# Performance work log

Hardware: AMD Instinct MI355X
Metric: run time of the kernel (lower is better)

Reference implementation:

```python
import jax, jax.numpy as jnp
import numpy as np

# Static part-graph structure (matches adj_matrix in init_kwargs; torch.nonzero row-major order)
ADJ = np.array([[0,1,0,0,0,0],
                [1,0,1,1,1,1],
                [0,1,0,0,0,0],
                [0,1,0,0,0,0],
                [0,1,0,0,0,0],
                [0,1,0,0,0,0]], dtype=np.int64)
_EDGES = np.argwhere(ADJ)            # [E,2] = (src, dst)
SRC = jnp.asarray(_EDGES[:, 0])
DST = jnp.asarray(_EDGES[:, 1])
NUM_PARTS = 6
# parts 1..4 are upper (use xh[0]), parts 5..6 lower (use xh[1])
HALVES = jnp.array([0, 0, 0, 0, 1, 1])


def setup_inputs() -> dict:
    key = jax.random.key(0)
    ks = jax.random.split(key, 12)
    B, H, W, Cin, h, P = 16, 96, 96, 256, 10, NUM_PARTS
    s = 0.05  # weight scale
    return {
        "p_fea":    jax.random.normal(ks[0], (B, Cin, H, W), jnp.float32),
        "xp_stack": jax.random.normal(ks[1], (P, B, h, H, W), jnp.float32),
        "xh_stack": jax.random.normal(ks[2], (2, B, h, H, W), jnp.float32),
        "w_att":  jax.random.normal(ks[3], (P, h), jnp.float32) * s,      # grouped 1x1 conv (groups=P)
        "b_att":  jnp.zeros((P,), jnp.float32),
        "w_dp_f": jax.random.normal(ks[4], (h, Cin), jnp.float32) * s,    # Part_Dependency: p_fea branch
        "w_dp_x": jax.random.normal(ks[5], (h, h), jnp.float32) * s,      # Part_Dependency: xp branch
        "b_dp":   jnp.zeros((h,), jnp.float32),
        "w_proj": jax.random.normal(ks[6], (P, h, Cin), jnp.float32) * s, # Decomposition proj (per part)
        "b_proj": jnp.zeros((P, h), jnp.float32),
        "w_gate": jax.random.normal(ks[7], (P, 2 * h), jnp.float32) * s,  # Decomposition gate on cat(xh,xp)
        "b_gate": jnp.zeros((P,), jnp.float32),
        "w_upd":  jax.random.normal(ks[8], (P, h, 3 * h), jnp.float32) * s,  # att_Update on cat(xp,xpp,xhp)
        "b_upd":  jnp.zeros((P, h), jnp.float32),
    }


def reference(p_fea, xp_stack, xh_stack, w_att, b_att, w_dp_f, w_dp_x, b_dp,
              w_proj, b_proj, w_gate, b_gate, w_upd, b_upd):
    # xp_stack: [P,B,h,H,W], p_fea: [B,Cin,H,W]
    P = xp_stack.shape[0]

    # grouped 1x1 conv + sigmoid -> per-part attention map [P,B,1,H,W]
    att = jax.nn.sigmoid(jnp.einsum('pbchw,pc->pbhw', xp_stack, w_att)
                         + b_att[:, None, None, None])[:, :, None]

    # Part_Dependency: dp_i = relu(W_f @ p_fea + W_x @ xp_i + b), shared weights -> [P,B,h,H,W]
    dp = jax.nn.relu(jnp.einsum('bchw,dc->bdhw', p_fea, w_dp_f)[None]
                     + jnp.einsum('pbchw,dc->pbdhw', xp_stack, w_dp_x)
                     + b_dp[None, None, :, None, None])

    # Pair_Part_Dependency per edge: sigmoid-gated fusion, then sum-aggregate at dst
    msg = att[SRC] * att[DST] * (dp[SRC] + xp_stack[DST])   # [E,B,h,H,W]
    xpp = jax.ops.segment_sum(msg, DST, num_segments=P)     # [P,B,h,H,W]

    # Decomposition: gate half-body feature onto a projection of p_fea (per-part weights)
    xh_sel = xh_stack[HALVES]                                # [P,B,h,H,W]
    proj = jnp.einsum('bchw,pdc->pbdhw', p_fea, w_proj) + b_proj[:, None, :, None, None]
    gate = jax.nn.sigmoid(jnp.einsum('pbchw,pc->pbhw',
                                     jnp.concatenate([xh_sel, xp_stack], axis=2), w_gate)
                          + b_gate[:, None, None, None])[:, :, None]
    xhp = gate * proj                                        # [P,B,h,H,W]

    # att_Update: residual update from cat(xp, xpp, xhp) via per-part 1x1 conv
    cat3 = jnp.concatenate([xp_stack, xpp, xhp], axis=2)     # [P,B,3h,H,W]
    xp_out = xp_stack + jax.nn.relu(jnp.einsum('pbchw,pdc->pbdhw', cat3, w_upd)
                                    + b_upd[:, None, :, None, None])
    return xp_out, xpp, xhp
```

## Files before the change

kernel.cpp:

```cpp
#include <hip/hip_runtime.h>

#define HWSZ 9216
#define CIN  256
#define NPER 8847360
#define PSTRIDE 1474560
#define IMG_STRIDE 2359296
#define BHW 92160

#define OFF_WATT  18432
#define OFF_BATT  18492
#define OFF_WDPX  18498
#define OFF_BDP   18598
#define OFF_BPROJ 18608
#define OFF_WGATE 18668
#define OFF_BGATE 18788
#define OFF_WUPD  18794
#define OFF_BUPD  20594
#define WS_TOTAL  20654
#define A_OFF_U16 41472
#define A_ELEMS   20480

typedef __attribute__((ext_vector_type(8))) short short8;
typedef __attribute__((ext_vector_type(4))) float f32x4;
typedef __attribute__((ext_vector_type(4))) float flt4;

static __device__ __forceinline__ unsigned short f2b(float f) {
  union { float f; unsigned int i; } v; v.f = f;
  unsigned int u = v.i;
  return (unsigned short)((u + 0x7fffu + ((u >> 16) & 1u)) >> 16);
}
static __device__ __forceinline__ float sigmoidf_(float x) {
  return 1.0f / (1.0f + __expf(-x));
}

__global__ void prep_weights(const float* __restrict__ w_att,
                             const float* __restrict__ b_att,
                             const float* __restrict__ w_dp_f,
                             const float* __restrict__ w_dp_x,
                             const float* __restrict__ b_dp,
                             const float* __restrict__ w_proj,
                             const float* __restrict__ b_proj,
                             const float* __restrict__ w_gate,
                             const float* __restrict__ b_gate,
                             const float* __restrict__ w_upd,
                             const float* __restrict__ b_upd,
                             float* __restrict__ ws)
{
  int i = blockIdx.x * 256 + threadIdx.x;
  if (i < A_ELEMS) {
    int j     = i & 7;
    int lane  = (i >> 3) & 63;
    int kstep = (i >> 9) & 7;
    int mtile = i >> 12;
    int m = mtile * 16 + (lane & 15);
    int k = kstep * 32 + ((lane >> 4) & 3) * 8 + j;
    float wv = (m < 10) ? w_dp_f[m * CIN + k]
             : (m < 70) ? w_proj[(m - 10) * CIN + k] : 0.f;
    ((unsigned short*)ws)[A_OFF_U16 + i] = f2b(wv);
  }
  if (i >= WS_TOTAL || i < OFF_WATT) return;
  float v;
  if      (i < OFF_BATT)  v = w_att [i - OFF_WATT ];
  else if (i < OFF_WDPX)  v = b_att [i - OFF_BATT ];
  else if (i < OFF_BDP)   v = w_dp_x[i - OFF_WDPX ];
  else if (i < OFF_BPROJ) v = b_dp  [i - OFF_BDP  ];
  else if (i < OFF_WGATE) v = b_proj[i - OFF_BPROJ];
  else if (i < OFF_BGATE) v = w_gate[i - OFF_WGATE];
  else if (i < OFF_WUPD)  v = b_gate[i - OFF_BGATE];
  else if (i < OFF_BUPD)  v = w_upd [i - OFF_WUPD ];
  else                    v = b_upd [i - OFF_BUPD ];
  ws[i] = v;
}

static __device__ __forceinline__ void epilogue1(
    int px, int p, int b, int s0,
    const float* __restrict__ xp, const float* __restrict__ xh,
    const float* __restrict__ ws,
    float* __restrict__ S, float* __restrict__ dpL,
    float* __restrict__ attL, float* __restrict__ gateL)
{
  const size_t base = (size_t)b * BHW + s0 + px;
  const float* xpb = xp + (size_t)p * PSTRIDE + base;
  const float* xhb = xh + (size_t)(p >= 4 ? 1 : 0) * PSTRIDE + base;
  float asum = ws[OFF_BATT + p], gsum = ws[OFF_BGATE + p];
  float xpv[10];
#pragma unroll
  for (int ch = 0; ch < 10; ++ch) {
    float x  = xpb[(size_t)ch * HWSZ];
    float hv = xhb[(size_t)ch * HWSZ];
    xpv[ch] = x;
    asum = fmaf(ws[OFF_WATT + p * 10 + ch], x, asum);
    gsum = fmaf(ws[OFF_WGATE + p * 20 + 10 + ch], x, gsum);
    gsum = fmaf(ws[OFF_WGATE + p * 20 + ch], hv, gsum);
  }
  attL [p * 64 + px] = sigmoidf_(asum);
  gateL[p * 64 + px] = sigmoidf_(gsum);
#pragma unroll
  for (int ch = 0; ch < 10; ++ch) {
    float t = S[ch * 72 + px] + ws[OFF_BDP + ch];
#pragma unroll
    for (int j = 0; j < 10; ++j) t = fmaf(ws[OFF_WDPX + ch * 10 + j], xpv[j], t);
    dpL[(p * 10 + ch) * 64 + px] = fmaxf(t, 0.f);
  }
}

static __device__ __forceinline__ void epilogue2(
    int px, int p, int b, int s0,
    const float* __restrict__ xp, const float* __restrict__ ws,
    const float* __restrict__ S, const float* __restrict__ dpL,
    const float* __restrict__ attL, const float* __restrict__ gateL,
    float* __restrict__ out)
{
  const size_t base = (size_t)b * BHW + s0 + px;
  const float* xpb = xp + (size_t)p * PSTRIDE + base;
  float xpv[10], xppv[10], xhpv[10];
#pragma unroll
  for (int ch = 0; ch < 10; ++ch) xpv[ch] = xpb[(size_t)ch * HWSZ];
  float att1 = attL[64 + px];
  if (p == 1) {
    float sA = 0.f;
#pragma unroll
    for (int q = 0; q < 6; ++q) if (q != 1) sA += attL[q * 64 + px];
#pragma unroll
    for (int ch = 0; ch < 10; ++ch) {
      float s1 = 0.f;
#pragma unroll
      for (int q = 0; q < 6; ++q)
        if (q != 1) s1 = fmaf(attL[q * 64 + px], dpL[(q * 10 + ch) * 64 + px], s1);
      xppv[ch] = att1 * fmaf(sA, xpv[ch], s1);
    }
  } else {
    float aa = att1 * attL[p * 64 + px];
#pragma unroll
    for (int ch = 0; ch < 10; ++ch)
      xppv[ch] = aa * (dpL[(10 + ch) * 64 + px] + xpv[ch]);
  }
  float g = gateL[p * 64 + px];
#pragma unroll
  for (int ch = 0; ch < 10; ++ch)
    xhpv[ch] = g * (S[(10 + p * 10 + ch) * 72 + px] + ws[OFF_BPROJ + p * 10 + ch]);
  float* o0 = out + (size_t)p * PSTRIDE + base;
#pragma unroll
  for (int ch = 0; ch < 10; ++ch) {
    float u = ws[OFF_BUPD + p * 10 + ch];
    const float* wu = ws + OFF_WUPD + (p * 10 + ch) * 30;
#pragma unroll
    for (int j = 0; j < 10; ++j) u = fmaf(wu[j],      xpv[j],  u);
#pragma unroll
    for (int j = 0; j < 10; ++j) u = fmaf(wu[10 + j], xppv[j], u);
#pragma unroll
    for (int j = 0; j < 10; ++j) u = fmaf(wu[20 + j], xhpv[j], u);
    u = fmaxf(u, 0.f);
    o0[(size_t)ch * HWSZ]                    = xpv[ch] + u;
    o0[(size_t)ch * HWSZ + NPER]             = xppv[ch];
    o0[(size_t)ch * HWSZ + 2 * (size_t)NPER] = xhpv[ch];
  }
}

__global__ __launch_bounds__(256) void part_graph_main(
    const float* __restrict__ p_fea,
    const float* __restrict__ xp,
    const float* __restrict__ xh,
    const float* __restrict__ ws,
    float* __restrict__ out)
{
  __shared__ __align__(16) char smem[38592];
  unsigned short* Bt = (unsigned short*)smem;
  float* S     = (float*)smem;
  float* dpL   = (float*)(smem + 20160);
  float* attL  = (float*)(smem + 35520);
  float* gateL = (float*)(smem + 37056);

  const int tid = threadIdx.x;
  const int b   = blockIdx.x / 144;
  const int s0  = (blockIdx.x % 144) * 64;

  {
    const int lane16 = tid & 15;
    const int cslot  = tid >> 4;
    const float* fb = p_fea + (size_t)b * IMG_STRIDE + s0 + lane16 * 4;
    const int nb = lane16 * 4;
#pragma unroll 4
    for (int it = 0; it < 16; ++it) {
      int c = cslot + it * 16;
      flt4 v = *(const flt4*)(fb + (size_t)c * HWSZ);
      Bt[(nb + 0) * 264 + c] = f2b(v.x);
      Bt[(nb + 1) * 264 + c] = f2b(v.y);
      Bt[(nb + 2) * 264 + c] = f2b(v.z);
      Bt[(nb + 3) * 264 + c] = f2b(v.w);
    }
  }
  __syncthreads();

  const int wv   = tid >> 6;
  const int lane = tid & 63;
  const int l15  = lane & 15;
  const int quad = lane >> 4;

  short8 bfrag[8];
  {
    const unsigned short* bp = Bt + (wv * 16 + l15) * 264 + quad * 8;
#pragma unroll
    for (int ks = 0; ks < 8; ++ks)
      bfrag[ks] = *(const short8*)(bp + ks * 32);
  }
  __syncthreads();

  f32x4 acc[5];
  const short8* ap = (const short8*)((const unsigned short*)ws + A_OFF_U16);
#pragma unroll
  for (int mt = 0; mt < 5; ++mt) {
    f32x4 a = {0.f, 0.f, 0.f, 0.f};
#pragma unroll
    for (int ks = 0; ks < 8; ++ks) {
      short8 af = ap[(mt * 8 + ks) * 64 + lane];
      a = __builtin_amdgcn_mfma_f32_16x16x32_bf16(af, bfrag[ks], a, 0, 0, 0);
    }
    acc[mt] = a;
  }

#pragma unroll
  for (int mt = 0; mt < 5; ++mt) {
#pragma unroll
    for (int r = 0; r < 4; ++r) {
      int m = mt * 16 + quad * 4 + r;
      if (m < 70) S[m * 72 + wv * 16 + l15] = acc[mt][r];
    }
  }
  __syncthreads();

  { int px = tid & 63, p = tid >> 6;
    epilogue1(px, p, b, s0, xp, xh, ws, S, dpL, attL, gateL); }
  if (tid < 128) {
    int px = tid & 63, p = 4 + (tid >> 6);
    epilogue1(px, p, b, s0, xp, xh, ws, S, dpL, attL, gateL);
  }
  __syncthreads();

  { int px = tid & 63, p = tid >> 6;
    epilogue2(px, p, b, s0, xp, ws, S, dpL, attL, gateL, out); }
  if (tid < 128) {
    int px = tid & 63, p = 4 + (tid >> 6);
    epilogue2(px, p, b, s0, xp, ws, S, dpL, attL, gateL, out);
  }
}

extern "C" void kernel_launch(void* const* d_in, const int* in_sizes, int n_in,
                              void* d_out, int out_size, void* d_ws, size_t ws_size,
                              hipStream_t stream) {
  const float* p_fea = (const float*)d_in[0];
  const float* xp    = (const float*)d_in[1];
  const float* xh    = (const float*)d_in[2];
  float* ws = (float*)d_ws;

  prep_weights<<<(WS_TOTAL + 255) / 256, 256, 0, stream>>>(
      (const float*)d_in[3],  (const float*)d_in[4],
      (const float*)d_in[5],  (const float*)d_in[6],
      (const float*)d_in[7],  (const float*)d_in[8],
      (const float*)d_in[9],  (const float*)d_in[10],
      (const float*)d_in[11], (const float*)d_in[12],
      (const float*)d_in[13], ws);

  part_graph_main<<<2304, 256, 0, stream>>>(
      p_fea, xp, xh, ws, (float*)d_out);
}
```

Baseline: 335.3 us.

## Load p_fea directly into MFMA fragments and restructure epilogue with paired pixels

Drops the shared-memory transpose of p_fea: each lane loads its B-fragment straight from global memory, converts it to bf16 and issues the MFMAs inline. The epilogue now has one thread handle two adjacent pixels for a single part, with 192 threads active. Each xp/xh value is loaded once and kept in registers across both phases instead of being re-read from global memory. The part-1 aggregation is reduced into shared memory with atomics rather than storing all per-part dp maps, which shrinks LDS and allows an occupancy hint of 6 blocks per SM. The risks are strided, uncoalesced global loads for the fragments, LDS atomics, and a quarter of the threads sitting idle in the epilogue.

After: 723.6 us. 116% more time.

```diff
diff --git a/kernel.cpp b/kernel.cpp
--- a/kernel.cpp
+++ b/kernel.cpp
@@ -22,7 +22,16 @@
 
 typedef __attribute__((ext_vector_type(8))) short short8;
 typedef __attribute__((ext_vector_type(4))) float f32x4;
-typedef __attribute__((ext_vector_type(4))) float flt4;
+typedef __attribute__((ext_vector_type(2))) float f32x2;
+
+#define SS     66
+#define L_S    0
+#define L_DP1  4620
+#define L_S1   5280
+#define L_SA   5940
+#define L_ATT  6008
+#define L_GATE 6392
+#define L_TOT  6776
 
 static __device__ __forceinline__ unsigned short f2b(float f) {
   union { float f; unsigned int i; } v; v.f = f;
@@ -72,151 +81,43 @@
   ws[i] = v;
 }
 
-static __device__ __forceinline__ void epilogue1(
-    int px, int p, int b, int s0,
-    const float* __restrict__ xp, const float* __restrict__ xh,
-    const float* __restrict__ ws,
-    float* __restrict__ S, float* __restrict__ dpL,
-    float* __restrict__ attL, float* __restrict__ gateL)
-{
-  const size_t base = (size_t)b * BHW + s0 + px;
-  const float* xpb = xp + (size_t)p * PSTRIDE + base;
-  const float* xhb = xh + (size_t)(p >= 4 ? 1 : 0) * PSTRIDE + base;
-  float asum = ws[OFF_BATT + p], gsum = ws[OFF_BGATE + p];
-  float xpv[10];
-#pragma unroll
-  for (int ch = 0; ch < 10; ++ch) {
-    float x  = xpb[(size_t)ch * HWSZ];
-    float hv = xhb[(size_t)ch * HWSZ];
-    xpv[ch] = x;
-    asum = fmaf(ws[OFF_WATT + p * 10 + ch], x, asum);
-    gsum = fmaf(ws[OFF_WGATE + p * 20 + 10 + ch], x, gsum);
-    gsum = fmaf(ws[OFF_WGATE + p * 20 + ch], hv, gsum);
-  }
-  attL [p * 64 + px] = sigmoidf_(asum);
-  gateL[p * 64 + px] = sigmoidf_(gsum);
-#pragma unroll
-  for (int ch = 0; ch < 10; ++ch) {
-    float t = S[ch * 72 + px] + ws[OFF_BDP + ch];
-#pragma unroll
-    for (int j = 0; j < 10; ++j) t = fmaf(ws[OFF_WDPX + ch * 10 + j], xpv[j], t);
-    dpL[(p * 10 + ch) * 64 + px] = fmaxf(t, 0.f);
-  }
-}
-
-static __device__ __forceinline__ void epilogue2(
-    int px, int p, int b, int s0,
-    const float* __restrict__ xp, const float* __restrict__ ws,
-    const float* __restrict__ S, const float* __restrict__ dpL,
-    const float* __restrict__ attL, const float* __restrict__ gateL,
-    float* __restrict__ out)
-{
-  const size_t base = (size_t)b * BHW + s0 + px;
-  const float* xpb = xp + (size_t)p * PSTRIDE + base;
-  float xpv[10], xppv[10], xhpv[10];
-#pragma unroll
-  for (int ch = 0; ch < 10; ++ch) xpv[ch] = xpb[(size_t)ch * HWSZ];
-  float att1 = attL[64 + px];
-  if (p == 1) {
-    float sA = 0.f;
-#pragma unroll
-    for (int q = 0; q < 6; ++q) if (q != 1) sA += attL[q * 64 + px];
-#pragma unroll
-    for (int ch = 0; ch < 10; ++ch) {
-      float s1 = 0.f;
-#pragma unroll
-      for (int q = 0; q < 6; ++q)
-        if (q != 1) s1 = fmaf(attL[q * 64 + px], dpL[(q * 10 + ch) * 64 + px], s1);
-      xppv[ch] = att1 * fmaf(sA, xpv[ch], s1);
-    }
-  } else {
-    float aa = att1 * attL[p * 64 + px];
-#pragma unroll
-    for (int ch = 0; ch < 10; ++ch)
-      xppv[ch] = aa * (dpL[(10 + ch) * 64 + px] + xpv[ch]);
-  }
-  float g = gateL[p * 64 + px];
-#pragma unroll
-  for (int ch = 0; ch < 10; ++ch)
-    xhpv[ch] = g * (S[(10 + p * 10 + ch) * 72 + px] + ws[OFF_BPROJ + p * 10 + ch]);
-  float* o0 = out + (size_t)p * PSTRIDE + base;
-#pragma unroll
-  for (int ch = 0; ch < 10; ++ch) {
-    float u = ws[OFF_BUPD + p * 10 + ch];
-    const float* wu = ws + OFF_WUPD + (p * 10 + ch) * 30;
-#pragma unroll
-    for (int j = 0; j < 10; ++j) u = fmaf(wu[j],      xpv[j],  u);
-#pragma unroll
-    for (int j = 0; j < 10; ++j) u = fmaf(wu[10 + j], xppv[j], u);
-#pragma unroll
-    for (int j = 0; j < 10; ++j) u = fmaf(wu[20 + j], xhpv[j], u);
-    u = fmaxf(u, 0.f);
-    o0[(size_t)ch * HWSZ]                    = xpv[ch] + u;
-    o0[(size_t)ch * HWSZ + NPER]             = xppv[ch];
-    o0[(size_t)ch * HWSZ + 2 * (size_t)NPER] = xhpv[ch];
-  }
-}
-
-__global__ __launch_bounds__(256) void part_graph_main(
+__global__ __launch_bounds__(256, 6) void part_graph_main(
     const float* __restrict__ p_fea,
     const float* __restrict__ xp,
     const float* __restrict__ xh,
     const float* __restrict__ ws,
     float* __restrict__ out)
 {
-  __shared__ __align__(16) char smem[38592];
-  unsigned short* Bt = (unsigned short*)smem;
-  float* S     = (float*)smem;
-  float* dpL   = (float*)(smem + 20160);
-  float* attL  = (float*)(smem + 35520);
-  float* gateL = (float*)(smem + 37056);
+  __shared__ __align__(16) float smem[L_TOT];
 
   const int tid = threadIdx.x;
   const int b   = blockIdx.x / 144;
   const int s0  = (blockIdx.x % 144) * 64;
 
-  {
-    const int lane16 = tid & 15;
-    const int cslot  = tid >> 4;
-    const float* fb = p_fea + (size_t)b * IMG_STRIDE + s0 + lane16 * 4;
-    const int nb = lane16 * 4;
-#pragma unroll 4
-    for (int it = 0; it < 16; ++it) {
-      int c = cslot + it * 16;
-      flt4 v = *(const flt4*)(fb + (size_t)c * HWSZ);
-      Bt[(nb + 0) * 264 + c] = f2b(v.x);
-      Bt[(nb + 1) * 264 + c] = f2b(v.y);
-      Bt[(nb + 2) * 264 + c] = f2b(v.z);
-      Bt[(nb + 3) * 264 + c] = f2b(v.w);
-    }
-  }
-  __syncthreads();
-
-  const int wv   = tid >> 6;
-  const int lane = tid & 63;
-  const int l15  = lane & 15;
-  const int quad = lane >> 4;
-
-  short8 bfrag[8];
-  {
-    const unsigned short* bp = Bt + (wv * 16 + l15) * 264 + quad * 8;
-#pragma unroll
-    for (int ks = 0; ks < 8; ++ks)
-      bfrag[ks] = *(const short8*)(bp + ks * 32);
-  }
-  __syncthreads();
+  for (int i = tid; i < 726; i += 256) smem[L_S1 + i] = 0.f;
+
+  const int lane = tid & 63, wv = tid >> 6;
+  const int l15  = lane & 15, quad = lane >> 4;
+  const float* pf = p_fea + (size_t)b * IMG_STRIDE + s0 + wv * 16 + l15
+                  + (size_t)quad * 8 * HWSZ;
+  const short8* ap = (const short8*)((const unsigned short*)ws + A_OFF_U16);
 
   f32x4 acc[5];
-  const short8* ap = (const short8*)((const unsigned short*)ws + A_OFF_U16);
-#pragma unroll
-  for (int mt = 0; mt < 5; ++mt) {
-    f32x4 a = {0.f, 0.f, 0.f, 0.f};
-#pragma unroll
-    for (int ks = 0; ks < 8; ++ks) {
-      short8 af = ap[(mt * 8 + ks) * 64 + lane];
-      a = __builtin_amdgcn_mfma_f32_16x16x32_bf16(af, bfrag[ks], a, 0, 0, 0);
-    }
-    acc[mt] = a;
+#pragma unroll
+  for (int mt = 0; mt < 5; ++mt) acc[mt] = (f32x4){0.f, 0.f, 0.f, 0.f};
+
+#pragma unroll
+  for (int ks = 0; ks < 8; ++ks) {
+    float t[8];
+#pragma unroll
+    for (int j = 0; j < 8; ++j) t[j] = pf[(size_t)(ks * 32 + j) * HWSZ];
+    short8 bf;
+#pragma unroll
+    for (int j = 0; j < 8; ++j) bf[j] = (short)f2b(t[j]);
+#pragma unroll
+    for (int mt = 0; mt < 5; ++mt)
+      acc[mt] = __builtin_amdgcn_mfma_f32_16x16x32_bf16(
+          ap[(mt * 8 + ks) * 64 + lane], bf, acc[mt], 0, 0, 0);
   }
 
 #pragma unroll
@@ -224,24 +125,137 @@
 #pragma unroll
     for (int r = 0; r < 4; ++r) {
       int m = mt * 16 + quad * 4 + r;
-      if (m < 70) S[m * 72 + wv * 16 + l15] = acc[mt][r];
+      if (m < 70) smem[L_S + m * SS + wv * 16 + l15] = acc[mt][r];
+    }
+  }
+
+  const int ep = tid >> 5;
+  const int px = (tid & 31) * 2;
+  const size_t ebase = (size_t)b * BHW + s0 + px;
+
+  f32x2 xp2[10], xh2[10];
+  if (tid < 192) {
+    const float* xpb = xp + (size_t)ep * PSTRIDE + ebase;
+    const float* xhb = xh + (size_t)(ep >= 4 ? 1 : 0) * PSTRIDE + ebase;
+#pragma unroll
+    for (int ch = 0; ch < 10; ++ch) {
+      xp2[ch] = *(const f32x2*)(xpb + (size_t)ch * HWSZ);
+      xh2[ch] = *(const f32x2*)(xhb + (size_t)ch * HWSZ);
     }
   }
   __syncthreads();
 
-  { int px = tid & 63, p = tid >> 6;
-    epilogue1(px, p, b, s0, xp, xh, ws, S, dpL, attL, gateL); }
-  if (tid < 128) {
-    int px = tid & 63, p = 4 + (tid >> 6);
-    epilogue1(px, p, b, s0, xp, xh, ws, S, dpL, attL, gateL);
+  if (tid < 192) {
+    float ba = ws[OFF_BATT + ep], bg = ws[OFF_BGATE + ep];
+    f32x2 asum = {ba, ba}, gsum = {bg, bg};
+#pragma unroll
+    for (int ch = 0; ch < 10; ++ch) {
+      float wa  = ws[OFF_WATT  + ep * 10 + ch];
+      float wgx = ws[OFF_WGATE + ep * 20 + 10 + ch];
+      float wgh = ws[OFF_WGATE + ep * 20 + ch];
+      asum.x = fmaf(wa,  xp2[ch].x, asum.x); asum.y = fmaf(wa,  xp2[ch].y, asum.y);
+      gsum.x = fmaf(wgx, xp2[ch].x, gsum.x); gsum.y = fmaf(wgx, xp2[ch].y, gsum.y);
+      gsum.x = fmaf(wgh, xh2[ch].x, gsum.x); gsum.y = fmaf(wgh, xh2[ch].y, gsum.y);
+    }
+    f32x2 att2, gate2;
+    att2.x  = sigmoidf_(asum.x); att2.y  = sigmoidf_(asum.y);
+    gate2.x = sigmoidf_(gsum.x); gate2.y = sigmoidf_(gsum.y);
+    *(f32x2*)&smem[L_ATT  + ep * 64 + px] = att2;
+    *(f32x2*)&smem[L_GATE + ep * 64 + px] = gate2;
+
+    if (ep == 1) {
+#pragma unroll
+      for (int ch = 0; ch < 10; ++ch) {
+        f32x2 t2 = *(const f32x2*)&smem[L_S + ch * SS + px];
+        float bd = ws[OFF_BDP + ch];
+        t2.x += bd; t2.y += bd;
+#pragma unroll
+        for (int j = 0; j < 10; ++j) {
+          float w = ws[OFF_WDPX + ch * 10 + j];
+          t2.x = fmaf(w, xp2[j].x, t2.x); t2.y = fmaf(w, xp2[j].y, t2.y);
+        }
+        t2.x = fmaxf(t2.x, 0.f); t2.y = fmaxf(t2.y, 0.f);
+        *(f32x2*)&smem[L_DP1 + ch * SS + px] = t2;
+      }
+    } else {
+#pragma unroll
+      for (int ch = 0; ch < 10; ++ch) {
+        f32x2 t2 = *(const f32x2*)&smem[L_S + ch * SS + px];
+        float bd = ws[OFF_BDP + ch];
+        t2.x += bd; t2.y += bd;
+#pragma unroll
+        for (int j = 0; j < 10; ++j) {
+          float w = ws[OFF_WDPX + ch * 10 + j];
+          t2.x = fmaf(w, xp2[j].x, t2.x); t2.y = fmaf(w, xp2[j].y, t2.y);
+        }
+        t2.x = fmaxf(t2.x, 0.f); t2.y = fmaxf(t2.y, 0.f);
+        atomicAdd(&smem[L_S1 + ch * SS + px],     att2.x * t2.x);
+        atomicAdd(&smem[L_S1 + ch * SS + px + 1], att2.y * t2.y);
+      }
+      atomicAdd(&smem[L_SA + px],     att2.x);
+      atomicAdd(&smem[L_SA + px + 1], att2.y);
+    }
   }
   __syncthreads();
 
-  { int px = tid & 63, p = tid >> 6;
-    epilogue2(px, p, b, s0, xp, ws, S, dpL, attL, gateL, out); }
-  if (tid < 128) {
-    int px = tid & 63, p = 4 + (tid >> 6);
-    epilogue2(px, p, b, s0, xp, ws, S, dpL, attL, gateL, out);
+  if (tid < 192) {
+    f32x2 att1 = *(const f32x2*)&smem[L_ATT + 64 + px];
+    f32x2 g2   = *(const f32x2*)&smem[L_GATE + ep * 64 + px];
+    f32x2 aa = {0.f, 0.f}, sa2 = {0.f, 0.f};
+    if (ep == 1) {
+      sa2 = *(const f32x2*)&smem[L_SA + px];
+    } else {
+      f32x2 ap2 = *(const f32x2*)&smem[L_ATT + ep * 64 + px];
+      aa.x = att1.x * ap2.x; aa.y = att1.y * ap2.y;
+    }
+
+    float* o0 = out + (size_t)ep * PSTRIDE + ebase;
+    const float* wu = ws + OFF_WUPD + ep * 300;
+
+    f32x2 u[10];
+#pragma unroll
+    for (int q = 0; q < 10; ++q) {
+      float bu = ws[OFF_BUPD + ep * 10 + q];
+      u[q].x = bu; u[q].y = bu;
+    }
+
+#pragma unroll
+    for (int ch = 0; ch < 10; ++ch) {
+      f32x2 xpp;
+      if (ep == 1) {
+        f32x2 s1v = *(const f32x2*)&smem[L_S1 + ch * SS + px];
+        xpp.x = att1.x * fmaf(sa2.x, xp2[ch].x, s1v.x);
+        xpp.y = att1.y * fmaf(sa2.y, xp2[ch].y, s1v.y);
+      } else {
+        f32x2 d1 = *(const f32x2*)&smem[L_DP1 + ch * SS + px];
+        xpp.x = aa.x * (d1.x + xp2[ch].x);
+        xpp.y = aa.y * (d1.y + xp2[ch].y);
+      }
+      f32x2 pr = *(const f32x2*)&smem[L_S + (10 + ep * 10 + ch) * SS + px];
+      float bp = ws[OFF_BPROJ + ep * 10 + ch];
+      f32x2 xhp;
+      xhp.x = g2.x * (pr.x + bp); xhp.y = g2.y * (pr.y + bp);
+
+      *(f32x2*)(o0 + (size_t)ch * HWSZ + NPER)             = xpp;
+      *(f32x2*)(o0 + (size_t)ch * HWSZ + 2 * (size_t)NPER) = xhp;
+
+#pragma unroll
+      for (int q = 0; q < 10; ++q) {
+        float w0 = wu[q * 30 + ch];
+        float w1 = wu[q * 30 + 10 + ch];
+        float w2 = wu[q * 30 + 20 + ch];
+        u[q].x = fmaf(w0, xp2[ch].x, u[q].x); u[q].y = fmaf(w0, xp2[ch].y, u[q].y);
+        u[q].x = fmaf(w1, xpp.x,     u[q].x); u[q].y = fmaf(w1, xpp.y,     u[q].y);
+        u[q].x = fmaf(w2, xhp.x,     u[q].x); u[q].y = fmaf(w2, xhp.y,     u[q].y);
+      }
+    }
+#pragma unroll
+    for (int q = 0; q < 10; ++q) {
+      f32x2 r;
+      r.x = xp2[q].x + fmaxf(u[q].x, 0.f);
+      r.y = xp2[q].y + fmaxf(u[q].y, 0.f);
+      *(f32x2*)(o0 + (size_t)q * HWSZ) = r;
+    }
   }
 }
 
```
